# Optimization experiments

Hardware: AMD Instinct MI355X
Metric: run time of the kernel (lower is better)

## Reference

```python
import jax, jax.numpy as jnp
import numpy as np
import math

L = 32            # one_side_length; seq_len = L*L = 1024
EMBED = 768
NDIM = 16
N_SSM = 768
DIRS = 4
K = DIRS * N_SSM  # kernel_dim = 3072
REPEAT = EMBED // N_SSM
SCALE = math.sqrt(1.0 / NDIM)


def _compute_kernel(A_angle, A_radius, B1p, B2p, C1p, C2p):
    # Polar-parameterized complex diagonal A's (4 transition coeffs), sigmoid B, raw C.
    ang = jax.nn.sigmoid(A_angle) * (2.0 * math.pi)
    rad = jax.nn.sigmoid(A_radius)
    A = (rad * jnp.cos(ang) + 1j * (rad * jnp.sin(ang))).astype(jnp.complex64)  # (4,K,NDIM)
    A1, A2, A3, A4 = A[0], A[1], A[2], A[3]
    sB1 = jax.nn.sigmoid(B1p); sB2 = jax.nn.sigmoid(B2p)
    B1 = (sB1[..., 0] + 1j * sB1[..., 1]).astype(jnp.complex64)   # (K,NDIM)
    B2 = (sB2[..., 0] + 1j * sB2[..., 1]).astype(jnp.complex64)
    C1 = (C1p[..., 0] + 1j * C1p[..., 1]).astype(jnp.complex64)
    C2 = (C2p[..., 0] + 1j * C2p[..., 1]).astype(jnp.complex64)

    zeros = jnp.zeros((L, K, NDIM), jnp.complex64)

    # 2-D SSM impulse response (same math the torch module precomputes via the
    # vandermonde / coefficient-table expansion):
    #   x_h[i,j] = A1 x_h[i,j-1] + A2 x_v[i,j-1] + B1 delta[i,j]
    #   x_v[i,j] = A3 x_h[i-1,j] + A4 x_v[i-1,j] + B2 delta[i,j]
    #   k[i,j]   = scale * Re(C1 . x_h[i,j] + C2 . x_v[i,j])
    def row_step(carry, i):
        xh_prev, xv_prev = carry                    # row i-1 states, (L,K,NDIM)
        first = (i == 0).astype(jnp.float32)
        xv = A3 * xh_prev + A4 * xv_prev            # vertical flow from row above
        xv = xv.at[0].add(first * B2)               # impulse at (0,0)
        h0 = (first * B1).astype(jnp.complex64)     # x_h[i,0]
        def col_step(h, v_left):
            h_new = A1 * h + A2 * v_left            # horizontal flow within the row
            return h_new, h_new
        _, xh_rest = jax.lax.scan(col_step, h0, xv[:-1])
        xh = jnp.concatenate([h0[None], xh_rest], axis=0)
        return (xh, xv), (xh, xv)

    (_, _), (XH, XV) = jax.lax.scan(row_step, (zeros, zeros), jnp.arange(L))
    # XH, XV: (L, L, K, NDIM) complex
    k = SCALE * (jnp.einsum('ijhn,hn->ijh', XH, C1) + jnp.einsum('ijhn,hn->ijh', XV, C2))
    # boundary corrections exactly as in the torch module
    k = k.at[0, :, :].multiply(2.0)
    k = k.at[:, 0, :].multiply(2.0)
    k = k.at[0, 0, :].divide(4.0)
    return k.real                                   # (L, L, K) float32


def _forward(x, A_angle, A_radius, B1p, B2p, C1p, C2p, omega):
    S, B, D = x.shape
    residual = x * omega
    k = _compute_kernel(A_angle, A_radius, B1p, B2p, C1p, C2p)
    k = jnp.transpose(k, (2, 0, 1))                 # (K, L, L)
    x4 = jnp.transpose(x, (1, 2, 0)).reshape(B, D, L, L)
    s2 = (2 * L, 2 * L)
    flips = [(), (-2,), (-1,), (-2, -1)]
    out = jnp.zeros((B, D, L, L), jnp.float32)
    for idx, fl in enumerate(flips):                # 4 scan directions via flips
        kk = jnp.tile(k[idx * N_SSM:(idx + 1) * N_SSM], (REPEAT, 1, 1))  # (D,L,L)
        xc = jnp.flip(x4, axis=fl) if fl else x4
        kf = jnp.fft.rfft2(kk, s=s2)
        xf = jnp.fft.rfft2(xc, s=s2)
        cur = jnp.fft.irfft2(xf * kf, s=s2)[..., :L, :L]
        out = out + (jnp.flip(cur, axis=fl) if fl else cur)
    out = jnp.transpose(out.reshape(B, D, S), (2, 0, 1))  # back to (S,B,D)
    return jax.nn.silu(out + residual)


def setup_inputs() -> dict:
    key = jax.random.key(0)
    ks = jax.random.split(key, 9)
    x = jax.random.normal(ks[0], (L * L, 16, EMBED), jnp.float32)
    A_angle = jax.random.uniform(ks[1], (4, K, NDIM), jnp.float32, 0.5, 3.0)
    A_radius = jax.random.uniform(ks[2], (4, K, NDIM), jnp.float32, 0.5, 3.0)
    B1p = 0.2 * jax.random.normal(ks[3], (K, NDIM, 2), jnp.float32)
    B2p = 0.2 * jax.random.normal(ks[4], (K, NDIM, 2), jnp.float32)
    C1p = jax.random.normal(ks[5], (K, NDIM, 2), jnp.float32)
    C2p = jax.random.normal(ks[6], (K, NDIM, 2), jnp.float32)
    omega = jax.random.normal(ks[7], (EMBED,), jnp.float32)
    return {"x": x, "A_angle": A_angle, "A_radius": A_radius, "B1p": B1p,
            "B2p": B2p, "C1p": C1p, "C2p": C2p, "omega": omega}


def reference(x, A_angle, A_radius, B1p, B2p, C1p, C2p, omega):
    return _forward(x, A_angle, A_radius, B1p, B2p, C1p, C2p, omega)
```

## Files before the change

kernel.cpp:

```cpp
#include <hip/hip_runtime.h>
#include <cmath>

#define TWO_PI 6.283185307179586476925f

typedef float f2 __attribute__((ext_vector_type(2)));

__device__ __forceinline__ float sigm(float v) { return 1.0f / (1.0f + __expf(-v)); }
__device__ __forceinline__ f2 mnegi(f2 v) { return (f2){v.y, -v.x}; }
__device__ __forceinline__ f2 mposi(f2 v) { return (f2){-v.y, v.x}; }
__device__ __forceinline__ f2 cmulf(f2 a, f2 b) {
    return (f2){a.x, a.x} * b + (f2){a.y, a.y} * mposi(b);
}
__device__ __forceinline__ f2 cms(f2 A, f2 v) {
    return (f2){A.x, A.x} * v + (f2){A.y, A.y} * (f2){-v.y, v.x};
}

template<int CTRL>
__device__ __forceinline__ float dpp0(float v) {
    return __int_as_float(__builtin_amdgcn_update_dpp(
        0, __float_as_int(v), CTRL, 0xf, 0xf, true));
}
template<int CTRL>
__device__ __forceinline__ f2 dpp2(f2 v) {
    return (f2){dpp0<CTRL>(v.x), dpp0<CTRL>(v.y)};
}
#define DPP_SHR1 0x111
#define DPP_SHR2 0x112
#define DPP_SHR4 0x114
#define DPP_ROR8 0x128

__device__ __forceinline__ float swz_xor16(float v) {
    return __int_as_float(__builtin_amdgcn_ds_swizzle(__float_as_int(v), 0x401F));
}

__device__ __forceinline__ int swz(int r, int c) {
    return (r << 6) | (c ^ ((r ^ (r << 3)) & 63));
}

__device__ __forceinline__ int gfidx(int o, int m, int c) {
    return o + (c << 3) + (m << 9);
}

template<bool INV, bool HALF, bool PRUNE>
__device__ __forceinline__ void dft8(f2* x) {
    const float RS = 0.70710678118654752440f;
    f2 t0, t1, t2, t3, t4, t5, t6, t7;
    if (HALF) {
        t0 = x[0]; t4 = x[0]; t1 = x[1]; t5 = x[1];
        t2 = x[2]; t6 = x[2]; t3 = x[3]; t7 = x[3];
    } else {
        t0 = x[0] + x[4]; t4 = x[0] - x[4];
        t1 = x[1] + x[5]; t5 = x[1] - x[5];
        t2 = x[2] + x[6]; t6 = x[2] - x[6];
        t3 = x[3] + x[7]; t7 = x[3] - x[7];
    }
    f2 t5w, t6w, t7w;
    if (!INV) {
        t5w = RS * (t5 + mnegi(t5));
        t6w = mnegi(t6);
        t7w = RS * (mnegi(t7) - t7);
    } else {
        t5w = RS * (t5 - mnegi(t5));
        t6w = mposi(t6);
        t7w = RS * (mposi(t7) - t7);
    }
    f2 u0 = t0 + t2, u2 = t0 - t2, u1 = t1 + t3, dd = t1 - t3;
    f2 u3 = INV ? mposi(dd) : mnegi(dd);
    x[0] = u0 + u1; x[2] = u2 + u3;
    if (!PRUNE) { x[4] = u0 - u1; x[6] = u2 - u3; }
    f2 v0 = t4 + t6w, v2 = t4 - t6w, v1 = t5w + t7w, ee = t5w - t7w;
    f2 v3 = INV ? mposi(ee) : mnegi(ee);
    x[1] = v0 + v1; x[3] = v2 + v3;
    if (!PRUNE) { x[5] = v0 - v1; x[7] = v2 - v3; }
}

__device__ __forceinline__ void make_tw(int o, f2* tw) {
    float s, co;
    __sincosf(-TWO_PI * (float)o / 64.f, &s, &co);
    tw[0] = (f2){co, s};
#pragma unroll
    for (int k = 1; k < 7; ++k) tw[k] = cmulf(tw[k - 1], tw[0]);
}

template<bool INV, bool COL, bool HALF, bool PRUNE>
__device__ __forceinline__ void fft64(f2* a, f2* r, const f2* tw,
                                      int o, int line) {
    dft8<INV, HALF, false>(r);
#pragma unroll
    for (int k = 1; k < 8; ++k) {
        f2 w = tw[k - 1];
        if (INV) w.y = -w.y;
        r[k] = cmulf(r[k], w);
    }
#pragma unroll
    for (int m = 0; m < 8; ++m) {
        int s = 8 * o + m;
        a[COL ? swz(s, line) : swz(line, s)] = r[m];
    }
#pragma unroll
    for (int j = 0; j < 8; ++j) {
        int s = 8 * j + o;
        r[j] = a[COL ? swz(s, line) : swz(line, s)];
    }
    dft8<INV, false, PRUNE>(r);
}

__global__ __launch_bounds__(512) void ssm_tin(
        const float* __restrict__ Aang, const float* __restrict__ Arad,
        const float* __restrict__ B1p, const float* __restrict__ B2p,
        const float* __restrict__ C1p, const float* __restrict__ C2p,
        f2* __restrict__ Gf, const float* __restrict__ x,
        float* __restrict__ xT) {
    __shared__ __align__(16) char smem[35840];
    int tid = threadIdx.x;

    if (blockIdx.x >= 768) {
        float (*tt)[65] = (float (*)[65])smem;
        int bb = blockIdx.x - 768;
        int bR = bb % 192, bS = bb / 192;
        int r0 = bR * 64, s0 = bS * 64;
        int c = tid & 63, w = tid >> 6;
#pragma unroll
        for (int k = 0; k < 8; ++k) {
            int row = w + 8 * k;
            tt[row][c] = x[(size_t)(s0 + row) * 12288 + r0 + c];
        }
        __syncthreads();
#pragma unroll
        for (int k = 0; k < 8; ++k) {
            int row = w + 8 * k;
            xT[(size_t)(r0 + row) * 1024 + s0 + c] = tt[c][row];
        }
        return;
    }

    f2* a = (f2*)smem;
    float* row0 = (float*)(smem + 32768);
    float* col0 = (float*)(smem + 34816);
    int d = blockIdx.x;
    int w = tid >> 6;
    int t = w & 3;
    int nh = w >> 2;
    int lane = tid & 63;
    int jg = lane & 7;
    int n8 = lane >> 3;
    int n = n8 + 8 * nh;
    int ch = t * 768 + d;
    int gid = ch * 16 + n;

    for (int e = tid; e < 4096; e += 512) a[e] = (f2){0.f, 0.f};
    row0[tid] = 0.f;
    if (tid < 256) col0[tid] = 0.f;

    f2 A[4];
#pragma unroll
    for (int q = 0; q < 4; ++q) {
        float ang = sigm(Aang[q * 49152 + gid]) * TWO_PI;
        float rad = sigm(Arad[q * 49152 + gid]);
        float s, co;
        __sincosf(ang, &s, &co);
        A[q] = (f2){rad * co, rad * s};
    }
    f2 A1 = A[0], A2 = A[1], A3 = A[2], A4 = A[3];
    f2 P2 = cms(A1, A1);
    f2 P3 = cms(A1, P2);
    f2 P4 = cms(P2, P2);
    f2 P8 = cms(P4, P4);
    f2 P16 = cms(P8, P8);
    f2 CZ1 = (jg >= 1) ? P4 : (f2){0.f, 0.f};
    f2 CZ2 = (jg >= 2) ? P8 : (f2){0.f, 0.f};
    f2 CZ4 = (jg >= 4) ? P16 : (f2){0.f, 0.f};

    const float2* B1v = (const float2*)B1p;
    const float2* B2v = (const float2*)B2p;
    const float2* C1v = (const float2*)C1p;
    const float2* C2v = (const float2*)C2p;
    float2 b1 = B1v[gid], b2 = B2v[gid], c1 = C1v[gid], c2 = C2v[gid];
    f2 B1 = (f2){sigm(b1.x), sigm(b1.y)};
    f2 B2 = (f2){sigm(b2.x), sigm(b2.y)};
    float c1r = c1.x, c1i = c1.y, c2r = c2.x, c2i = c2.y;

    f2 pw = (f2){1.f, 0.f};
    if (jg & 1) pw = P4;
    if (jg & 2) pw = cms(pw, P8);
    if (jg & 4) pw = cms(pw, P16);
    f2 EB = cms(pw, B1);

    int bb0 = n8 & 1, bb1 = (n8 >> 1) & 1;
    int col = 4 * jg + 2 * bb0 + bb1;
    int ccl = (t & 2) ? ((64 - col) & 63) : col;

    __syncthreads();

    f2 xv[4], xh[4];
#pragma unroll
    for (int m = 0; m < 4; ++m) { xv[m] = (f2){0.f, 0.f}; xh[m] = (f2){0.f, 0.f}; }

    auto body = [&](int i, bool is0) {
#pragma unroll
        for (int m = 0; m < 4; ++m) xv[m] = cms(A3, xh[m]) + cms(A4, xv[m]);
        if (is0 && jg == 0) xv[0] += B2;
        f2 g1 = cms(A2, xv[0]);
        f2 g2 = cms(A1, g1) + cms(A2, xv[1]);
        f2 g3 = cms(A1, g2) + cms(A2, xv[2]);
        f2 V  = cms(A1, g3) + cms(A2, xv[3]);
        V += cms(CZ1, dpp2<DPP_SHR1>(V));
        V += cms(CZ2, dpp2<DPP_SHR2>(V));
        V += cms(CZ4, dpp2<DPP_SHR4>(V));
        f2 E = dpp2<DPP_SHR1>(V);
        if (jg == 0) E = (f2){0.f, 0.f};
        if (is0) E += EB;
        xh[0] = E;
        xh[1] = cms(A1, E) + g1;
        xh[2] = cms(P2, E) + g2;
        xh[3] = cms(P3, E) + g3;
        float v0 = c1r * xh[0].x - c1i * xh[0].y + c2r * xv[0].x - c2i * xv[0].y;
        float v1 = c1r * xh[1].x - c1i * xh[1].y + c2r * xv[1].x - c2i * xv[1].y;
        float v2 = c1r * xh[2].x - c1i * xh[2].y + c2r * xv[2].x - c2i * xv[2].y;
        float v3 = c1r * xh[3].x - c1i * xh[3].y + c2r * xv[3].x - c2i * xv[3].y;
        float s0 = bb0 ? v0 : v2, s1 = bb0 ? v1 : v3;
        float r0 = dpp0<DPP_ROR8>(s0), r1 = dpp0<DPP_ROR8>(s1);
        float q0 = (bb0 ? v2 : v0) + r0;
        float q1 = (bb0 ? v3 : v1) + r1;
        float s2 = bb1 ? q0 : q1;
        float r2 = swz_xor16(s2);
        float qq = (bb1 ? q1 : q0) + r2;
        qq += __shfl_xor(qq, 32, 64);
        if (n8 < 4) {
            if (is0) {
                row0[(((t << 1) | nh) << 6) | ccl] = qq;
            } else if (col == 0) {
                col0[((((t >> 1) << 1) | nh) << 6) | ((t & 1) ? (64 - i) : i)] = qq;
            } else {
                int rr_ = (t & 1) ? (64 - i) : i;
                ((float*)&a[swz(rr_, ccl)])[nh] = qq;
            }
        }
    };
    body(0, true);
#pragma unroll 1
    for (int i = 1; i < 32; ++i) body(i, false);

    __syncthreads();
    for (int e = tid; e < 4096; e += 512) {
        int r = e >> 6, cm = e & 63;
        int c = cm ^ ((r ^ (r << 3)) & 63);
        f2 cv = a[e];
        float v = cv.x + cv.y;
        if (r == 0) {
            v += row0[c] + row0[64 + c] + row0[128 + c] + row0[192 + c]
               + row0[256 + c] + row0[320 + c] + row0[384 + c] + row0[448 + c];
        } else if (c == 0) {
            v += col0[r] + col0[64 + r] + col0[128 + r] + col0[192 + r];
        }
        float f = 0.25f;
        if (r == 0) f *= 2.f;
        if (c == 0) f *= 2.f;
        if (r == 0 && c == 0) f *= 0.25f;
        a[e] = (f2){f * v, 0.f};
    }
    __syncthreads();
    int o = tid & 7;
    f2 tw[7];
    make_tw(o, tw);
    {
        int row = tid >> 3;
        f2 r[8];
#pragma unroll
        for (int j = 0; j < 8; ++j) r[j] = a[swz(row, 8 * j + o)];
        fft64<false, false, false, false>(a, r, tw, o, row);
#pragma unroll
        for (int m = 0; m < 8; ++m) a[swz(row, o + 8 * m)] = r[m];
    }
    __syncthreads();
    {
        int cc = tid >> 3;
        f2 r[8];
#pragma unroll
        for (int j = 0; j < 8; ++j) r[j] = a[swz(8 * j + o, cc)];
        fft64<false, true, false, false>(a, r, tw, o, cc);
#pragma unroll
        for (int m = 0; m < 8; ++m) Gf[d * 4096 + gfidx(o, m, cc)] = r[m];
    }
}

__global__ __launch_bounds__(512) void conv_fft(
        const float* __restrict__ x, float* __restrict__ xT,
        const f2* __restrict__ Gf, const float* __restrict__ omega,
        float* __restrict__ out, int useT) {
    __shared__ f2 a[4096];
    int bid = (blockIdx.x & 7) * 768 + (blockIdx.x >> 3);
    int d = bid >> 3, b = (bid & 7) * 2;
    int tid = threadIdx.x;
    int o = tid & 7, grp = tid >> 3;
    f2 tw[7];
    make_tw(o, tw);
    const size_t base0 = (size_t)(b * 768 + d) * 1024;
    const size_t base1 = (size_t)((b + 1) * 768 + d) * 1024;
    f2 xsave[4];
    if (grp < 32) {
        int row = grp;
        f2 r[8];
#pragma unroll
        for (int j = 0; j < 4; ++j) {
            int s2 = row * 32 + 8 * j + o;
            if (useT) r[j] = (f2){xT[base0 + s2], xT[base1 + s2]};
            else      r[j] = (f2){x[s2 * 12288 + b * 768 + d],
                                  x[s2 * 12288 + (b + 1) * 768 + d]};
            xsave[j] = r[j];
        }
#pragma unroll
        for (int j = 4; j < 8; ++j) r[j] = (f2){0.f, 0.f};
        fft64<false, false, true, false>(a, r, tw, o, row);
#pragma unroll
        for (int m = 0; m < 8; ++m) a[swz(row, o + 8 * m)] = r[m];
    }
    __syncthreads();
    {
        int c = grp;
        f2 r[8];
#pragma unroll
        for (int j = 0; j < 4; ++j) r[j] = a[swz(8 * j + o, c)];
#pragma unroll
        for (int j = 4; j < 8; ++j) r[j] = (f2){0.f, 0.f};
        fft64<false, true, true, false>(a, r, tw, o, c);
#pragma unroll
        for (int m = 0; m < 8; ++m) {
            r[m] = cmulf(r[m], Gf[d * 4096 + gfidx(o, m, c)]);
        }
        fft64<true, true, false, true>(a, r, tw, o, c);
#pragma unroll
        for (int m = 0; m < 4; ++m) a[swz(o + 8 * m, c)] = r[m];
    }
    __syncthreads();
    if (grp < 32) {
        int row = grp;
        f2 r[8];
#pragma unroll
        for (int j = 0; j < 8; ++j) r[j] = a[swz(row, 8 * j + o)];
        fft64<true, false, false, true>(a, r, tw, o, row);
        float w = omega[d];
        const float inv = 1.0f / 4096.0f;
#pragma unroll
        for (int m = 0; m < 4; ++m) {
            int cc = o + 8 * m;
            int s2 = row * 32 + cc;
            float xa = xsave[m].x, xb = xsave[m].y;
            float ya = r[m].x * inv + xa * w;
            float yb = r[m].y * inv + xb * w;
            float oa = ya / (1.0f + __expf(-ya));
            float ob = yb / (1.0f + __expf(-yb));
            if (useT) {
                xT[base0 + s2] = oa;
                xT[base1 + s2] = ob;
            } else {
                out[s2 * 12288 + b * 768 + d] = oa;
                out[s2 * 12288 + (b + 1) * 768 + d] = ob;
            }
        }
    }
}

__global__ __launch_bounds__(256) void transpose_out(const float* __restrict__ xT,
                                                     float* __restrict__ out) {
    __shared__ float t[64][65];
    int bR = blockIdx.x % 192, bS = blockIdx.x / 192;
    int r0 = bR * 64, s0 = bS * 64;
    int c = threadIdx.x & 63, w = threadIdx.x >> 6;
#pragma unroll
    for (int k = 0; k < 16; ++k) {
        int row = w + 4 * k;
        t[row][c] = xT[(size_t)(r0 + row) * 1024 + s0 + c];
    }
    __syncthreads();
#pragma unroll
    for (int k = 0; k < 16; ++k) {
        int row = w + 4 * k;
        out[(size_t)(s0 + row) * 12288 + r0 + c] = t[c][row];
    }
}

extern "C" void kernel_launch(void* const* d_in, const int* in_sizes, int n_in,
                              void* d_out, int out_size, void* d_ws, size_t ws_size,
                              hipStream_t stream) {
    const float* x     = (const float*)d_in[0];
    const float* Aang  = (const float*)d_in[1];
    const float* Arad  = (const float*)d_in[2];
    const float* B1p   = (const float*)d_in[3];
    const float* B2p   = (const float*)d_in[4];
    const float* C1p   = (const float*)d_in[5];
    const float* C2p   = (const float*)d_in[6];
    const float* omega = (const float*)d_in[7];
    float* out = (float*)d_out;
    char* ws = (char*)d_ws;

    f2*    Gf = (f2*)ws;
    float* xT = (float*)(ws + 25165824);
    int useT = (ws_size >= (size_t)75497472) ? 1 : 0;

    int grid1 = useT ? 3840 : 768;
    ssm_tin<<<grid1, 512, 0, stream>>>(Aang, Arad, B1p, B2p, C1p, C2p, Gf, x, xT);
    conv_fft<<<6144, 512, 0, stream>>>(x, xT, Gf, omega, out, useT);
    if (useT) transpose_out<<<3072, 256, 0, stream>>>(xT, out);
}
```

Baseline: 147.5 us.

## Vectorize transposes with float4, reorder Gf layout, unroll scan, raise occupancy

Both transpose paths (inside ssm_tin and transpose_out) now move data with float4 global loads and stores instead of scalar ones. The frequency-domain kernel buffer Gf switches to a layout where each thread's eight values for a column are contiguous, so reads in conv_fft are better localised. The row-scan loop is unrolled by two, and conv_fft gets a minimum-waves-per-EU launch bound to push occupancy. The transposes pick up some LDS bank conflicts from strided column reads, and the occupancy hint may force register spills.

Result: slower. 300.5 us (+103.8%).

```diff
diff --git a/kernel.cpp b/kernel.cpp
--- a/kernel.cpp
+++ b/kernel.cpp
@@ -37,8 +37,8 @@
     return (r << 6) | (c ^ ((r ^ (r << 3)) & 63));
 }
 
-__device__ __forceinline__ int gfidx(int o, int m, int c) {
-    return o + (c << 3) + (m << 9);
+__device__ __forceinline__ int gfx2(int o, int m, int c) {
+    return (c << 6) | (o << 3) | m;
 }
 
 template<bool INV, bool HALF, bool PRUNE>
@@ -119,17 +119,20 @@
         int bb = blockIdx.x - 768;
         int bR = bb % 192, bS = bb / 192;
         int r0 = bR * 64, s0 = bS * 64;
-        int c = tid & 63, w = tid >> 6;
-#pragma unroll
-        for (int k = 0; k < 8; ++k) {
-            int row = w + 8 * k;
-            tt[row][c] = x[(size_t)(s0 + row) * 12288 + r0 + c];
+        int c4 = (tid & 15) * 4, rw = tid >> 4;
+#pragma unroll
+        for (int k = 0; k < 2; ++k) {
+            int row = rw + 32 * k;
+            float4 v = *(const float4*)&x[(size_t)(s0 + row) * 12288 + r0 + c4];
+            tt[row][c4] = v.x; tt[row][c4 + 1] = v.y;
+            tt[row][c4 + 2] = v.z; tt[row][c4 + 3] = v.w;
         }
         __syncthreads();
 #pragma unroll
-        for (int k = 0; k < 8; ++k) {
-            int row = w + 8 * k;
-            xT[(size_t)(r0 + row) * 1024 + s0 + c] = tt[c][row];
+        for (int k = 0; k < 2; ++k) {
+            int row = rw + 32 * k;
+            float4 v = {tt[c4][row], tt[c4 + 1][row], tt[c4 + 2][row], tt[c4 + 3][row]};
+            *(float4*)&xT[(size_t)(r0 + row) * 1024 + s0 + c4] = v;
         }
         return;
     }
@@ -238,7 +241,7 @@
         }
     };
     body(0, true);
-#pragma unroll 1
+#pragma unroll 2
     for (int i = 1; i < 32; ++i) body(i, false);
 
     __syncthreads();
@@ -279,12 +282,13 @@
 #pragma unroll
         for (int j = 0; j < 8; ++j) r[j] = a[swz(8 * j + o, cc)];
         fft64<false, true, false, false>(a, r, tw, o, cc);
-#pragma unroll
-        for (int m = 0; m < 8; ++m) Gf[d * 4096 + gfidx(o, m, cc)] = r[m];
-    }
-}
-
-__global__ __launch_bounds__(512) void conv_fft(
+        f2* GfD = Gf + d * 4096;
+#pragma unroll
+        for (int m = 0; m < 8; ++m) GfD[gfx2(o, m, cc)] = r[m];
+    }
+}
+
+__global__ __launch_bounds__(512, 8) void conv_fft(
         const float* __restrict__ x, float* __restrict__ xT,
         const f2* __restrict__ Gf, const float* __restrict__ omega,
         float* __restrict__ out, int useT) {
@@ -318,6 +322,7 @@
     __syncthreads();
     {
         int c = grp;
+        const f2* GfD = Gf + d * 4096;
         f2 r[8];
 #pragma unroll
         for (int j = 0; j < 4; ++j) r[j] = a[swz(8 * j + o, c)];
@@ -326,7 +331,7 @@
         fft64<false, true, true, false>(a, r, tw, o, c);
 #pragma unroll
         for (int m = 0; m < 8; ++m) {
-            r[m] = cmulf(r[m], Gf[d * 4096 + gfidx(o, m, c)]);
+            r[m] = cmulf(r[m], GfD[gfx2(o, m, c)]);
         }
         fft64<true, true, false, true>(a, r, tw, o, c);
 #pragma unroll
@@ -366,17 +371,20 @@
     __shared__ float t[64][65];
     int bR = blockIdx.x % 192, bS = blockIdx.x / 192;
     int r0 = bR * 64, s0 = bS * 64;
-    int c = threadIdx.x & 63, w = threadIdx.x >> 6;
-#pragma unroll
-    for (int k = 0; k < 16; ++k) {
-        int row = w + 4 * k;
-        t[row][c] = xT[(size_t)(r0 + row) * 1024 + s0 + c];
-    }
-    __syncthreads();
-#pragma unroll
-    for (int k = 0; k < 16; ++k) {
-        int row = w + 4 * k;
-        out[(size_t)(s0 + row) * 12288 + r0 + c] = t[c][row];
+    int c4 = (threadIdx.x & 15) * 4, rw = threadIdx.x >> 4;
+#pragma unroll
+    for (int k = 0; k < 4; ++k) {
+        int row = rw + 16 * k;
+        float4 v = *(const float4*)&xT[(size_t)(r0 + row) * 1024 + s0 + c4];
+        t[row][c4] = v.x; t[row][c4 + 1] = v.y;
+        t[row][c4 + 2] = v.z; t[row][c4 + 3] = v.w;
+    }
+    __syncthreads();
+#pragma unroll
+    for (int k = 0; k < 4; ++k) {
+        int row = rw + 16 * k;
+        float4 v = {t[c4][row], t[c4 + 1][row], t[c4 + 2][row], t[c4 + 3][row]};
+        *(float4*)&out[(size_t)(s0 + row) * 12288 + r0 + c4] = v;
     }
 }
 
```
